# Performance work log

Hardware: AMD Instinct MI355X
Metric: run time of the kernel (lower is better)

## Reference

```python
import jax, jax.numpy as jnp
import numpy as np

B, S, D_MODEL, N_HEADS, D_HEAD = 2, 2048, 512, 8, 64
AMBIENT_K = -1.0
EPS = 1e-7


def log_map_origin(x, K):
    """Lorentz log map at origin, curvature K<0. x: (..., d+1) -> (..., d)."""
    c = -K
    sc = jnp.sqrt(c)
    x_t = x[..., :1]
    x_s = x[..., 1:]
    nrm = jnp.maximum(jnp.linalg.norm(x_s, axis=-1, keepdims=True), EPS)
    theta = jnp.arccosh(jnp.maximum(sc * x_t, 1.0 + EPS)) / sc  # geodesic distance
    return theta * x_s / nrm


def exp_map_batched(u, K_vals):
    """Per-head Lorentz exp map at origin. u: (B,S,H,dh), K_vals: (H,) negative.
    Returns (B,S,H,dh+1) with time component first."""
    c = (-K_vals)[None, None, :, None]          # (1,1,H,1)
    sc = jnp.sqrt(c)
    n = jnp.maximum(jnp.linalg.norm(u, axis=-1, keepdims=True), EPS)
    t = jnp.cosh(sc * n) / sc                   # time component
    s = jnp.sinh(sc * n) / (sc * n) * u         # space components
    return jnp.concatenate([t, s], axis=-1)


def setup_inputs() -> dict:
    key = jax.random.key(0)
    k_x, k_q, k_k, k_v, k_o = jax.random.split(key, 5)
    # Lorentz points on the K=-1 manifold: x_t = sqrt(1 + |x_s|^2)
    x_s = 0.5 * jax.random.normal(k_x, (B, S, D_MODEL), dtype=jnp.float32)
    x_t = jnp.sqrt(1.0 + jnp.sum(x_s * x_s, axis=-1, keepdims=True))
    x = jnp.concatenate([x_t, x_s], axis=-1)    # (B, S, d_model+1)
    scale = 1.0 / np.sqrt(D_MODEL)
    W_q = scale * jax.random.normal(k_q, (D_MODEL, N_HEADS * D_HEAD), dtype=jnp.float32)
    W_k = scale * jax.random.normal(k_k, (D_MODEL, N_HEADS * D_HEAD), dtype=jnp.float32)
    W_v = scale * jax.random.normal(k_v, (D_MODEL, N_HEADS * D_HEAD), dtype=jnp.float32)
    W_o = scale * jax.random.normal(k_o, (N_HEADS * D_HEAD, D_MODEL), dtype=jnp.float32)
    log_abs_K = jnp.zeros((N_HEADS,), dtype=jnp.float32)  # init_K = -1 -> log(1) = 0
    return {"x": x, "W_q": W_q, "W_k": W_k, "W_v": W_v, "W_o": W_o,
            "log_abs_K": log_abs_K}


def reference(x, W_q, W_k, W_v, W_o, log_abs_K):
    b, s, _ = x.shape
    K_vals = -jnp.exp(log_abs_K)                            # (H,) negative curvatures
    x_eu = log_map_origin(x, AMBIENT_K)                     # (B,S,D)
    Q = (x_eu @ W_q).reshape(b, s, N_HEADS, D_HEAD)
    Kp = (x_eu @ W_k).reshape(b, s, N_HEADS, D_HEAD)
    V = (x_eu @ W_v).reshape(b, s, N_HEADS, D_HEAD)
    Q_hyp = exp_map_batched(Q, K_vals).transpose(0, 2, 1, 3)   # (B,H,S,dh+1)
    K_hyp = exp_map_batched(Kp, K_vals).transpose(0, 2, 1, 3)
    V = V.transpose(0, 2, 1, 3)                                # (B,H,S,dh)
    Q_t, Q_s = Q_hyp[..., 0], Q_hyp[..., 1:]
    K_t, K_s = K_hyp[..., 0], K_hyp[..., 1:]
    # Lorentzian inner product: -q_t k_t + <q_s, k_s>
    lorentz_ip = (jnp.einsum('bhqd,bhkd->bhqk', Q_s, K_s)
                  - jnp.einsum('bhq,bhk->bhqk', Q_t, K_t))
    abs_K = jnp.exp(log_abs_K)[None, :, None, None]
    scores = abs_K * (-lorentz_ip) / np.sqrt(D_HEAD)           # (B,H,S,S)
    causal = jnp.triu(jnp.ones((s, s), dtype=bool), k=1)[None, None]
    scores = jnp.where(causal, -jnp.inf, scores)
    attn = jax.nn.softmax(scores, axis=-1)
    out = jnp.einsum('bhqk,bhkd->bhqd', attn, V)               # (B,H,S,dh)
    out = out.transpose(0, 2, 1, 3).reshape(b, s, N_HEADS * D_HEAD)
    return out @ W_o                                           # (B,S,D)
```

## Files before the change

### kernel.cpp

```cpp
#include <hip/hip_runtime.h>
#include <math.h>

#define S_LEN 2048
#define B_SZ 2
#define NH 8
#define DH 64
#define DM 512
#define MROWS 4096

typedef __attribute__((ext_vector_type(8))) short s16x8;
typedef __attribute__((ext_vector_type(4))) float fx4;
typedef __attribute__((ext_vector_type(16))) float fx16;
typedef __attribute__((ext_vector_type(4))) int ix4;
typedef __attribute__((ext_vector_type(2))) int ix2;

__device__ inline short f2bf(float x){
  unsigned u = __float_as_uint(x);
  u = (u + 0x7FFFu + ((u >> 16) & 1u)) >> 16;
  return (short)u;
}
__device__ inline float bf2f(short s){
  return __uint_as_float(((unsigned)(unsigned short)s) << 16);
}

__device__ inline fx4 mfma16(s16x8 a, s16x8 b, fx4 c){
  return __builtin_amdgcn_mfma_f32_16x16x32_bf16(a, b, c, 0, 0, 0);
}
__device__ inline fx16 mfma32(s16x8 a, s16x8 b, fx16 c){
  return __builtin_amdgcn_mfma_f32_32x32x16_bf16(a, b, c, 0, 0, 0);
}
__device__ inline int cvtpk(float a, float b){
  int r; asm("v_cvt_pk_bf16_f32 %0, %1, %2" : "=v"(r) : "v"(a), "v"(b)); return r;
}

#define GLL16(g, l) __builtin_amdgcn_global_load_lds((const __attribute__((address_space(1))) void*)(g), (__attribute__((address_space(3))) void*)(l), 16, 0, 0)
#define GLL4(g, l)  __builtin_amdgcn_global_load_lds((const __attribute__((address_space(1))) void*)(g), (__attribute__((address_space(3))) void*)(l), 4, 0, 0)

__global__ __launch_bounds__(256) void prep_kernel(const float* __restrict__ W0,
                                                   const float* __restrict__ W1,
                                                   const float* __restrict__ W2,
                                                   const float* __restrict__ W3,
                                                   short* __restrict__ Wt,
                                                   const float* __restrict__ x,
                                                   short* __restrict__ xeu){
  __shared__ short tile[64][66];
  int bid = blockIdx.x;
  int t = threadIdx.x;
  if (bid < 256){
    int z = bid >> 6, rem = bid & 63;
    const float* W = (z == 0) ? W0 : (z == 1) ? W1 : (z == 2) ? W2 : W3;
    short* Wtz = Wt + (size_t)z * DM * DM;
    int n0 = (rem & 7) * 64, k0 = (rem >> 3) * 64;
    int nl = t & 63;
    #pragma unroll
    for (int p = 0; p < 16; ++p){
      int kl = (t >> 6) + p * 4;
      tile[kl][nl] = f2bf(W[(size_t)(k0 + kl) * DM + n0 + nl]);
    }
    __syncthreads();
    int kl2 = t & 63;
    #pragma unroll
    for (int p = 0; p < 16; ++p){
      int nl2 = (t >> 6) + p * 4;
      Wtz[(size_t)(n0 + nl2) * DM + k0 + kl2] = tile[kl2][nl2];
    }
  } else {
    int row = (bid - 256) * 4 + (t >> 6);
    int lane = t & 63;
    const float* xr = x + (size_t)row * (DM + 1);
    float v[8]; float ss = 0.f;
    #pragma unroll
    for (int j = 0; j < 8; ++j){
      v[j] = xr[1 + lane * 8 + j];
      ss += v[j] * v[j];
    }
    #pragma unroll
    for (int off = 1; off < 64; off <<= 1) ss += __shfl_xor(ss, off);
    float nrm = sqrtf(ss);
    float xt = xr[0];
    float theta = acoshf(fmaxf(xt, 1.0f + 1e-7f));
    float scl = theta / fmaxf(nrm, 1e-7f);
    s16x8 pk;
    #pragma unroll
    for (int j = 0; j < 8; ++j) pk[j] = f2bf(scl * v[j]);
    *(s16x8*)(xeu + (size_t)row * DM + lane * 8) = pk;
  }
}

__global__ __launch_bounds__(256, 2) void gemm_fused_kernel(const short* __restrict__ A,
                                                            const short* __restrict__ Bt,
                                                            const float* __restrict__ labsK,
                                                            float* __restrict__ Qt,
                                                            short* __restrict__ Qs,
                                                            float* __restrict__ Kt,
                                                            short* __restrict__ Ks,
                                                            short* __restrict__ Vt){
  __shared__ __attribute__((aligned(16))) short Stage[4][8192];
  const int K = DM;
  int z = blockIdx.z;
  int hp = blockIdx.y;
  int n0 = hp * 128, m0 = blockIdx.x * 128;
  int t = threadIdx.x;
  int w = t >> 6, lane = t & 63;
  int wm = w >> 1, wn = w & 1;
  int lg = lane >> 4, lr = lane & 15;
  const short* Btz = Bt + (size_t)z * K * DM;

  int coff[4]; const short* asrcp[4]; const short* bsrcp[4];
  #pragma unroll
  for (int j = 0; j < 4; ++j){
    int ch = t + 256 * j;
    int r = ch >> 3, c = ch & 7;
    coff[j] = ch * 8;
    asrcp[j] = A   + (size_t)(m0 + r) * K + 8 * (c ^ (r & 7));
    bsrcp[j] = Btz + (size_t)(n0 + r) * K + 8 * (c ^ (r & 7));
  }

  #pragma unroll
  for (int j = 0; j < 4; ++j){
    GLL16(asrcp[j], &Stage[0][coff[j]]);
    GLL16(bsrcp[j], &Stage[2][coff[j]]);
  }

  fx4 acc[4][4] = {};
  for (int ks = 0; ks < 4; ++ks){
    ;
    break;
  }
  for (int ks = 0; ks < 8; ++ks){
    asm volatile("s_waitcnt vmcnt(0)" ::: "memory");
    __builtin_amdgcn_s_barrier();
    if (ks < 7){
      int nb = (ks + 1) & 1;
      int kk = (ks + 1) * 64;
      #pragma unroll
      for (int j = 0; j < 4; ++j){
        GLL16(asrcp[j] + kk, &Stage[nb][coff[j]]);
        GLL16(bsrcp[j] + kk, &Stage[2 + nb][coff[j]]);
      }
    }
    int buf = ks & 1;
    s16x8 af[4][2], bf[4][2];
    #pragma unroll
    for (int mi = 0; mi < 4; ++mi){
      int row = wm * 64 + mi * 16 + lr;
      #pragma unroll
      for (int s = 0; s < 2; ++s)
        af[mi][s] = *(const s16x8*)&Stage[buf][row * 64 + ((4 * s + lg) ^ (row & 7)) * 8];
    }
    #pragma unroll
    for (int ni = 0; ni < 4; ++ni){
      int row = wn * 64 + ni * 16 + lr;
      #pragma unroll
      for (int s = 0; s < 2; ++s)
        bf[ni][s] = *(const s16x8*)&Stage[2 + buf][row * 64 + ((4 * s + lg) ^ (row & 7)) * 8];
    }
    __builtin_amdgcn_s_setprio(1);
    #pragma unroll
    for (int s = 0; s < 2; ++s)
      #pragma unroll
      for (int mi = 0; mi < 4; ++mi)
        #pragma unroll
        for (int ni = 0; ni < 4; ++ni)
          acc[mi][ni] = mfma16(af[mi][s], bf[ni][s], acc[mi][ni]);
    __builtin_amdgcn_s_setprio(0);
  }

  int h = hp * 2 + wn;
  if (z < 2){
    float c  = __expf(labsK[h]);
    float sc = sqrtf(c);
    float invsc = __frcp_rn(sc);
    float a  = 0.125f * c * 1.4426950408889634f;
    float tmul = (z == 0) ? a : 1.0f;
    float vmul = (z == 0) ? -a : 1.0f;
    float* Tt = (z == 0) ? Qt : Kt;
    short* Ts = (z == 0) ? Qs : Ks;
    #pragma unroll
    for (int mi = 0; mi < 4; ++mi)
      #pragma unroll
      for (int r = 0; r < 4; ++r){
        float prt = 0.f;
        #pragma unroll
        for (int ni = 0; ni < 4; ++ni) prt += acc[mi][ni][r] * acc[mi][ni][r];
        prt += __shfl_xor(prt, 1);
        prt += __shfl_xor(prt, 2);
        prt += __shfl_xor(prt, 4);
        prt += __shfl_xor(prt, 8);
        float n = fmaxf(sqrtf(prt), 1e-7f);
        float arg = sc * n;
        float e = __expf(arg), ei = __frcp_rn(e);
        float tval = tmul * 0.5f * (e + ei) * invsc;
        float vscl = vmul * 0.5f * (e - ei) * __frcp_rn(arg);
        int grow = m0 + wm * 64 + mi * 16 + 4 * lg + r;
        int b = grow >> 11, s = grow & (S_LEN - 1);
        size_t bhs = ((size_t)(b * NH + h) * S_LEN + s);
        if (lr == 0) Tt[bhs] = tval;
        #pragma unroll
        for (int ni = 0; ni < 4; ++ni)
          Ts[bhs * DH + ni * 16 + lr] = f2bf(vscl * acc[mi][ni][r]);
      }
  } else {
    __syncthreads();
    short* vt = &Stage[0][0] + w * 4352;
    #pragma unroll
    for (int mi = 0; mi < 4; ++mi)
      #pragma unroll
      for (int ni = 0; ni < 4; ++ni)
        #pragma unroll
        for (int r = 0; r < 4; ++r)
          vt[(ni * 16 + lr) * 68 + mi * 16 + 4 * lg + r] = f2bf(acc[mi][ni][r]);
    int b = m0 >> 11;
    int sglob = (m0 & (S_LEN - 1)) + wm * 64;
    size_t vbase = ((size_t)(b * NH + h) * DH + lane) * S_LEN + sglob;
    #pragma unroll
    for (int j = 0; j < 8; ++j){
      s16x8 val = *(const s16x8*)&vt[lane * 68 + j * 8];
      *(s16x8*)(Vt + vbase + j * 8) = val;
    }
  }
}

__global__ __launch_bounds__(256, 3) void attn_kernel(const short* __restrict__ Qs,
                                                      const float* __restrict__ Qt,
                                                      const short* __restrict__ Ks,
                                                      const float* __restrict__ Kt,
                                                      const short* __restrict__ Vt,
                                                      float* __restrict__ Mpart,
                                                      float* __restrict__ Lpart,
                                                      short* __restrict__ Obn,
                                                      short* __restrict__ Obf){
  __shared__ __attribute__((aligned(16))) short Ksm[3][4096];
  __shared__ __attribute__((aligned(16))) short Vsm[3][4096];
  __shared__ __attribute__((aligned(16))) float Ktm[3][64];

  int bx = blockIdx.x;
  int bh = bx & 15;
  int id = bx >> 4;
  int g, c;
  if (id < 4)       { g = id;                 c = 0; }
  else if (id < 12) { g = 4 + ((id - 4) >> 1);  c = (id - 4) & 1; }
  else if (id < 24) { int r = id - 12; int q3 = r / 3; g = 8 + q3; c = r - 3 * q3; }
  else              { g = 12 + ((id - 24) >> 2); c = (id - 24) & 3; }
  int nch = (g >> 2) + 1;
  int kbeg = 512 * c;
  int kend = 512 * c + 512; { int ge = 128 * g + 128; if (ge < kend) kend = ge; }
  int ntc = (kend - kbeg) >> 6;

  int tid = threadIdx.x;
  int w = tid >> 6, lane = tid & 63;
  int l5 = lane & 31, hi = lane >> 5;
  size_t bhS = (size_t)bh * S_LEN;

  const short* Kg  = Ks + bhS * DH;
  const short* Vg  = Vt + (size_t)bh * DH * S_LEN;
  const float* Ktg = Kt + bhS;

  int srow = lane >> 3;
  int scol = ((lane & 7) * 8) ^ (srow << 3);
  const short* kg0 = Kg + (size_t)(kbeg + 16 * w + srow) * DH + scol;
  const short* kg1 = kg0 + 8 * DH;
  const short* vg0 = Vg + (size_t)(16 * w + srow) * S_LEN + kbeg + scol;
  const short* vg1 = vg0 + 8 * S_LEN;
  const float* ktg = Ktg + kbeg + lane;

  int q0w = 128 * g + 32 * w;
  int q   = q0w + l5;
  int qmax = q0w + 31;
  s16x8 qf[4];
  #pragma unroll
  for (int dblk = 0; dblk < 4; ++dblk)
    qf[dblk] = *(const s16x8*)(Qs + (bhS + q) * DH + dblk * 16 + hi * 8);
  float aqt = Qt[bhS + q];

  fx16 acc0, acc1;
  #pragma unroll
  for (int i = 0; i < 16; ++i){ acc0[i] = 0.f; acc1[i] = 0.f; }
  float mrun = 0.f, lrun = 0.f;

  #define STAGE_T(tt, b) { int off_ = (tt) * 64; \
    GLL16(kg0 + (size_t)off_ * DH, &Ksm[b][16 * w * 64]); \
    GLL16(kg1 + (size_t)off_ * DH, &Ksm[b][16 * w * 64 + 512]); \
    GLL16(vg0 + off_, &Vsm[b][16 * w * 64]); \
    GLL16(vg1 + off_, &Vsm[b][16 * w * 64 + 512]); \
    if (w == 3) GLL4(ktg + off_, &Ktm[b][0]); }

  STAGE_T(0, 0);
  if (ntc > 1) STAGE_T(1, 1);

  int buf = 0, sbuf = 2;
  for (int t = 0; t < ntc; ++t){
    int k0 = kbeg + t * 64;
    if (t + 1 < ntc){
      if (w == 3) asm volatile("s_waitcnt vmcnt(5)" ::: "memory");
      else        asm volatile("s_waitcnt vmcnt(4)" ::: "memory");
    } else {
      asm volatile("s_waitcnt vmcnt(0)" ::: "memory");
    }
    __builtin_amdgcn_s_barrier();
    if (t + 2 < ntc) STAGE_T(t + 2, sbuf);

    if (k0 <= qmax){
      fx16 st[2];
      __builtin_amdgcn_s_setprio(1);
      #pragma unroll
      for (int s = 0; s < 2; ++s){
        const short* kb = &Ksm[buf][(32 * s + l5) * 64];
        fx16 z;
        #pragma unroll
        for (int i = 0; i < 16; ++i) z[i] = 0.f;
        #pragma unroll
        for (int dblk = 0; dblk < 4; ++dblk){
          s16x8 kf = *(const s16x8*)(kb + ((16 * dblk + 8 * hi) ^ ((l5 & 7) << 3)));
          z = mfma32(kf, qf[dblk], z);
        }
        st[s] = z;
      }
      __builtin_amdgcn_s_setprio(0);
      float p[2][16];
      #pragma unroll
      for (int s = 0; s < 2; ++s)
        #pragma unroll
        for (int m4 = 0; m4 < 4; ++m4){
          fx4 kt4 = *(const fx4*)&Ktm[buf][32 * s + 8 * m4 + 4 * hi];
          #pragma unroll
          for (int tt = 0; tt < 4; ++tt)
            p[s][4 * m4 + tt] = st[s][4 * m4 + tt] + aqt * kt4[tt];
        }
      if (k0 + 63 > q0w){
        #pragma unroll
        for (int s = 0; s < 2; ++s)
          #pragma unroll
          for (int r = 0; r < 16; ++r){
            int kg2 = k0 + 32 * s + (r & 3) + 8 * (r >> 2) + 4 * hi;
            if (kg2 > q) p[s][r] = -3e38f;
          }
      }
      float v16[16];
      #pragma unroll
      for (int i = 0; i < 16; ++i) v16[i] = fmaxf(p[0][i], p[1][i]);
      #pragma unroll
      for (int i = 0; i < 8; ++i) v16[i] = fmaxf(v16[i], v16[i + 8]);
      #pragma unroll
      for (int i = 0; i < 4; ++i) v16[i] = fmaxf(v16[i], v16[i + 4]);
      float pmax = fmaxf(fmaxf(v16[0], v16[1]), fmaxf(v16[2], v16[3]));
      pmax = fmaxf(pmax, __shfl_xor(pmax, 32));
      if (!__all(pmax <= mrun + 8.f)){
        float mnew = fmaxf(mrun, pmax);
        float scl = __builtin_amdgcn_exp2f(mrun - mnew);
        mrun = mnew;
        lrun *= scl;
        #pragma unroll
        for (int i = 0; i < 16; ++i){ acc0[i] *= scl; acc1[i] *= scl; }
      }
      float sm[16];
      #pragma unroll
      for (int i = 0; i < 16; ++i){
        p[0][i] = __builtin_amdgcn_exp2f(p[0][i] - mrun);
        p[1][i] = __builtin_amdgcn_exp2f(p[1][i] - mrun);
        sm[i] = p[0][i] + p[1][i];
      }
      #pragma unroll
      for (int i = 0; i < 8; ++i) sm[i] += sm[i + 8];
      #pragma unroll
      for (int i = 0; i < 4; ++i) sm[i] += sm[i + 4];
      float rsum = (sm[0] + sm[1]) + (sm[2] + sm[3]);
      rsum += __shfl_xor(rsum, 32);
      lrun += rsum;

      #pragma unroll
      for (int h = 0; h < 4; ++h){
        int s = h >> 1, hb = h & 1;
        int w0 = cvtpk(p[s][8 * hb + 0], p[s][8 * hb + 1]);
        int w1 = cvtpk(p[s][8 * hb + 2], p[s][8 * hb + 3]);
        int w2 = cvtpk(p[s][8 * hb + 4], p[s][8 * hb + 5]);
        int w3 = cvtpk(p[s][8 * hb + 6], p[s][8 * hb + 7]);
        int sdA = hi ? w0 : w2;
        int sdB = hi ? w1 : w3;
        int rcA = __shfl_xor(sdA, 32);
        int rcB = __shfl_xor(sdB, 32);
        ix4 fw;
        fw.x = hi ? rcA : w0; fw.y = hi ? rcB : w1;
        fw.z = hi ? w2 : rcA; fw.w = hi ? w3 : rcB;
        s16x8 pf = __builtin_bit_cast(s16x8, fw);
        const short* vb0 = &Vsm[buf][(l5) * 64 + ((16 * h + 8 * hi) ^ ((l5 & 7) << 3))];
        const short* vb1 = vb0 + 32 * 64;
        s16x8 vf0 = *(const s16x8*)vb0;
        s16x8 vf1 = *(const s16x8*)vb1;
        __builtin_amdgcn_s_setprio(1);
        acc0 = mfma32(vf0, pf, acc0);
        acc1 = mfma32(vf1, pf, acc1);
        __builtin_amdgcn_s_setprio(0);
      }
    }
    buf  = (buf == 2)  ? 0 : buf + 1;
    sbuf = (sbuf == 2) ? 0 : sbuf + 1;
  }

  float invl = 1.0f / lrun;
  int qi = 32 * w + l5;
  if (nch == 1){
    int bb = bh >> 3, hh = bh & 7;
    short* orow = Obf + ((size_t)bb * S_LEN + 128 * g + qi) * DM + hh * DH;
    #pragma unroll
    for (int j = 0; j < 4; ++j){
      ix2 v0, v1;
      v0.x = cvtpk(acc0[4 * j + 0] * invl, acc0[4 * j + 1] * invl);
      v0.y = cvtpk(acc0[4 * j + 2] * invl, acc0[4 * j + 3] * invl);
      v1.x = cvtpk(acc1[4 * j + 0] * invl, acc1[4 * j + 1] * invl);
      v1.y = cvtpk(acc1[4 * j + 2] * invl, acc1[4 * j + 3] * invl);
      *(ix2*)(orow + 8 * j + 4 * hi)      = v0;
      *(ix2*)(orow + 32 + 8 * j + 4 * hi) = v1;
    }
  } else {
    int slot = ((bh << 4) + g) * 4 + c;
    if (hi == 0){
      Mpart[(size_t)slot * 128 + qi] = mrun;
      Lpart[(size_t)slot * 128 + qi] = lrun;
    }
    short* Op = Obn + (size_t)slot * 8192 + (size_t)qi * 64;
    #pragma unroll
    for (int j = 0; j < 4; ++j){
      ix2 v0, v1;
      v0.x = cvtpk(acc0[4 * j + 0] * invl, acc0[4 * j + 1] * invl);
      v0.y = cvtpk(acc0[4 * j + 2] * invl, acc0[4 * j + 3] * invl);
      v1.x = cvtpk(acc1[4 * j + 0] * invl, acc1[4 * j + 1] * invl);
      v1.y = cvtpk(acc1[4 * j + 2] * invl, acc1[4 * j + 3] * invl);
      *(ix2*)(Op + 8 * j + 4 * hi)      = v0;
      *(ix2*)(Op + 32 + 8 * j + 4 * hi) = v1;
    }
  }
}

__global__ __launch_bounds__(256) void combine_kernel(const float* __restrict__ Mpart,
                                                      const float* __restrict__ Lpart,
                                                      const short* __restrict__ Obn,
                                                      short* __restrict__ Obf){
  int bx = blockIdx.x;
  int bhg = bx % 192;
  int qq = bx / 192;
  int bh = bhg & 15;
  int g = 4 + (bhg >> 4);
  int t = threadIdx.x;
  int q = qq * 32 + (t >> 3);
  int oct = t & 7;
  int nch = (g >> 2) + 1;
  int gbase = ((bh << 4) + g) * 4;

  float mc[4], lc[4];
  #pragma unroll
  for (int c = 0; c < 4; ++c){
    mc[c] = Mpart[(size_t)(gbase + c) * 128 + q];
    lc[c] = Lpart[(size_t)(gbase + c) * 128 + q];
    if (c >= nch) mc[c] = -3e38f;
  }
  float M = fmaxf(fmaxf(mc[0], mc[1]), fmaxf(mc[2], mc[3]));
  float ww[4]; float D = 0.f;
  #pragma unroll
  for (int c = 0; c < 4; ++c){
    ww[c] = __builtin_amdgcn_exp2f(mc[c] - M) * lc[c];
    if (c >= nch) ww[c] = 0.f;
    D += ww[c];
  }
  float invD = 1.f / D;
  #pragma unroll
  for (int c = 0; c < 4; ++c) ww[c] *= invD;

  const short* ob = Obn + (size_t)gbase * 8192 + (size_t)q * 64 + oct * 8;
  float accf[8] = {0.f,0.f,0.f,0.f,0.f,0.f,0.f,0.f};
  #pragma unroll
  for (int c = 0; c < 4; ++c){
    s16x8 v = *(const s16x8*)(ob + (size_t)c * 8192);
    #pragma unroll
    for (int i = 0; i < 8; ++i) accf[i] += ww[c] * bf2f(v[i]);
  }
  s16x8 pk;
  #pragma unroll
  for (int dd = 0; dd < 8; ++dd) pk[dd] = f2bf(accf[dd]);
  int bb = bh >> 3, hh = bh & 7;
  *(s16x8*)(Obf + ((size_t)bb * S_LEN + 128 * g + q) * DM + hh * DH + oct * 8) = pk;
}

__global__ __launch_bounds__(256, 4) void gemm_o_kernel(const short* __restrict__ A,
                                                        const short* __restrict__ Bt,
                                                        float* __restrict__ C){
  __shared__ __attribute__((aligned(16))) short Asm[2][64 * 64];
  __shared__ __attribute__((aligned(16))) short Bsm[2][64 * 64];
  const int K = DM;
  int n0 = blockIdx.y * 64, m0 = blockIdx.x * 64;
  int t = threadIdx.x;
  int w = t >> 6, lane = t & 63;
  int wm = w >> 1, wn = w & 1;
  int lg = lane >> 4, lr = lane & 15;

  int aoff[2]; const short* asrcp[2];
  int boff[2]; const short* bsrcp[2];
  #pragma unroll
  for (int j = 0; j < 2; ++j){
    int ch = t + 256 * j;
    int r = ch >> 3, c = ch & 7;
    aoff[j] = ch * 8;
    asrcp[j] = A + (size_t)(m0 + r) * K + 8 * (c ^ (r & 7));
    boff[j] = ch * 8;
    bsrcp[j] = Bt + (size_t)(n0 + r) * K + 8 * (c ^ (r & 7));
  }

  {
    short* ab = &Asm[0][0]; short* bb = &Bsm[0][0];
    #pragma unroll
    for (int j = 0; j < 2; ++j){ GLL16(asrcp[j], ab + aoff[j]); GLL16(bsrcp[j], bb + boff[j]); }
  }

  fx4 acc[2][2] = {};
  for (int ks = 0; ks < 8; ++ks){
    asm volatile("s_waitcnt vmcnt(0)" ::: "memory");
    __builtin_amdgcn_s_barrier();
    if (ks < 7){
      int nb = (ks + 1) & 1;
      short* ab = &Asm[nb][0]; short* bb = &Bsm[nb][0];
      int kk = (ks + 1) * 64;
      #pragma unroll
      for (int j = 0; j < 2; ++j){ GLL16(asrcp[j] + kk, ab + aoff[j]); GLL16(bsrcp[j] + kk, bb + boff[j]); }
    }
    int buf = ks & 1;
    s16x8 af[2][2], bf[2][2];
    #pragma unroll
    for (int mi = 0; mi < 2; ++mi){
      int row = wm * 32 + mi * 16 + lr;
      #pragma unroll
      for (int s = 0; s < 2; ++s)
        af[mi][s] = *(const s16x8*)&Asm[buf][row * 64 + ((4 * s + lg) ^ (row & 7)) * 8];
    }
    #pragma unroll
    for (int ni = 0; ni < 2; ++ni){
      int row = wn * 32 + ni * 16 + lr;
      #pragma unroll
      for (int s = 0; s < 2; ++s)
        bf[ni][s] = *(const s16x8*)&Bsm[buf][row * 64 + ((4 * s + lg) ^ (row & 7)) * 8];
    }
    __builtin_amdgcn_s_setprio(1);
    #pragma unroll
    for (int s = 0; s < 2; ++s)
      #pragma unroll
      for (int mi = 0; mi < 2; ++mi)
        #pragma unroll
        for (int ni = 0; ni < 2; ++ni)
          acc[mi][ni] = mfma16(af[mi][s], bf[ni][s], acc[mi][ni]);
    __builtin_amdgcn_s_setprio(0);
  }

  #pragma unroll
  for (int mi = 0; mi < 2; ++mi)
    #pragma unroll
    for (int ni = 0; ni < 2; ++ni)
      #pragma unroll
      for (int r = 0; r < 4; ++r){
        int row = m0 + wm * 32 + mi * 16 + 4 * lg + r;
        int col = n0 + wn * 32 + ni * 16 + lr;
        C[(size_t)row * DM + col] = acc[mi][ni][r];
      }
}

extern "C" void kernel_launch(void* const* d_in, const int* in_sizes, int n_in,
                              void* d_out, int out_size, void* d_ws, size_t ws_size,
                              hipStream_t stream) {
  const float* x     = (const float*)d_in[0];
  const float* Wq    = (const float*)d_in[1];
  const float* Wk    = (const float*)d_in[2];
  const float* Wv    = (const float*)d_in[3];
  const float* Wo    = (const float*)d_in[4];
  const float* labsK = (const float*)d_in[5];

  char* w = (char*)d_ws;
  short* Wt    = (short*)(w);
  short* xeu   = (short*)(w + (2ull  << 20));
  short* Qs    = (short*)(w + (30ull << 20));
  short* Ks    = (short*)(w + (34ull << 20));
  short* Vt    = (short*)(w + (38ull << 20));
  float* Qt    = (float*)(w + (42ull << 20));
  float* Kt    = (float*)(w + (42ull << 20) + (128ull << 10));
  short* Obf   = (short*)(w + (42ull << 20) + (256ull << 10));
  short* Obn   = (short*)(w + (48ull << 20));
  float* Mpart = (float*)(w + (80ull << 20));
  float* Lpart = (float*)(w + (81ull << 20));

  prep_kernel<<<dim3(1280), 256, 0, stream>>>(Wq, Wk, Wv, Wo, Wt, x, xeu);

  gemm_fused_kernel<<<dim3(32, 4, 3), 256, 0, stream>>>(
      xeu, Wt, labsK, Qt, Qs, Kt, Ks, Vt);

  attn_kernel<<<dim3(640), 256, 0, stream>>>(
      Qs, Qt, Ks, Kt, Vt, Mpart, Lpart, Obn, Obf);

  combine_kernel<<<dim3(768), 256, 0, stream>>>(Mpart, Lpart, Obn, Obf);

  gemm_o_kernel<<<dim3(64, 8), 256, 0, stream>>>(Obf, Wt + 3 * DM * DM, (float*)d_out);
}
```

Before: 59.86 us.

## Replace split-K attention plus combine with 64-query blocks scheduled longest-first

The attention kernel no longer splits long causal rows into key chunks with partial max/sum outputs merged by a separate combine kernel. Each block now has 128 threads (2 waves) handling 64 queries over all causal key tiles, with blocks ordered so the longest query groups launch first. This removes the combine launch and the partial-result global traffic, at the cost of longer serial loops for late query blocks and less parallelism per row. The new block size also doubles the K/V staging loads per wave and changes the wait counts to match.

```diff
diff --git a/kernel.cpp b/kernel.cpp
--- a/kernel.cpp
+++ b/kernel.cpp
@@ -18,9 +18,6 @@
   unsigned u = __float_as_uint(x);
   u = (u + 0x7FFFu + ((u >> 16) & 1u)) >> 16;
   return (short)u;
-}
-__device__ inline float bf2f(short s){
-  return __uint_as_float(((unsigned)(unsigned short)s) << 16);
 }
 
 __device__ inline fx4 mfma16(s16x8 a, s16x8 b, fx4 c){
@@ -77,8 +74,7 @@
     #pragma unroll
     for (int off = 1; off < 64; off <<= 1) ss += __shfl_xor(ss, off);
     float nrm = sqrtf(ss);
-    float xt = xr[0];
-    float theta = acoshf(fmaxf(xt, 1.0f + 1e-7f));
+    float theta = acoshf(fmaxf(xr[0], 1.0f + 1e-7f));
     float scl = theta / fmaxf(nrm, 1e-7f);
     s16x8 pk;
     #pragma unroll
@@ -123,10 +119,6 @@
   }
 
   fx4 acc[4][4] = {};
-  for (int ks = 0; ks < 4; ++ks){
-    ;
-    break;
-  }
   for (int ks = 0; ks < 8; ++ks){
     asm volatile("s_waitcnt vmcnt(0)" ::: "memory");
     __builtin_amdgcn_s_barrier();
@@ -221,14 +213,11 @@
   }
 }
 
-__global__ __launch_bounds__(256, 3) void attn_kernel(const short* __restrict__ Qs,
+__global__ __launch_bounds__(128, 2) void attn_kernel(const short* __restrict__ Qs,
                                                       const float* __restrict__ Qt,
                                                       const short* __restrict__ Ks,
                                                       const float* __restrict__ Kt,
                                                       const short* __restrict__ Vt,
-                                                      float* __restrict__ Mpart,
-                                                      float* __restrict__ Lpart,
-                                                      short* __restrict__ Obn,
                                                       short* __restrict__ Obf){
   __shared__ __attribute__((aligned(16))) short Ksm[3][4096];
   __shared__ __attribute__((aligned(16))) short Vsm[3][4096];
@@ -236,16 +225,8 @@
 
   int bx = blockIdx.x;
   int bh = bx & 15;
-  int id = bx >> 4;
-  int g, c;
-  if (id < 4)       { g = id;                 c = 0; }
-  else if (id < 12) { g = 4 + ((id - 4) >> 1);  c = (id - 4) & 1; }
-  else if (id < 24) { int r = id - 12; int q3 = r / 3; g = 8 + q3; c = r - 3 * q3; }
-  else              { g = 12 + ((id - 24) >> 2); c = (id - 24) & 3; }
-  int nch = (g >> 2) + 1;
-  int kbeg = 512 * c;
-  int kend = 512 * c + 512; { int ge = 128 * g + 128; if (ge < kend) kend = ge; }
-  int ntc = (kend - kbeg) >> 6;
+  int g  = 31 - (bx >> 4);
+  int ntc = g + 1;
 
   int tid = threadIdx.x;
   int w = tid >> 6, lane = tid & 63;
@@ -258,15 +239,12 @@
 
   int srow = lane >> 3;
   int scol = ((lane & 7) * 8) ^ (srow << 3);
-  const short* kg0 = Kg + (size_t)(kbeg + 16 * w + srow) * DH + scol;
-  const short* kg1 = kg0 + 8 * DH;
-  const short* vg0 = Vg + (size_t)(16 * w + srow) * S_LEN + kbeg + scol;
-  const short* vg1 = vg0 + 8 * S_LEN;
-  const float* ktg = Ktg + kbeg + lane;
-
-  int q0w = 128 * g + 32 * w;
+  const short* kgA = Kg + (size_t)(32 * w + srow) * DH + scol;
+  const short* vgA = Vg + (size_t)(32 * w + srow) * S_LEN + scol;
+  const float* ktg = Ktg + lane;
+
+  int q0w = 64 * g + 32 * w;
   int q   = q0w + l5;
-  int qmax = q0w + 31;
   s16x8 qf[4];
   #pragma unroll
   for (int dblk = 0; dblk < 4; ++dblk)
@@ -279,28 +257,32 @@
   float mrun = 0.f, lrun = 0.f;
 
   #define STAGE_T(tt, b) { int off_ = (tt) * 64; \
-    GLL16(kg0 + (size_t)off_ * DH, &Ksm[b][16 * w * 64]); \
-    GLL16(kg1 + (size_t)off_ * DH, &Ksm[b][16 * w * 64 + 512]); \
-    GLL16(vg0 + off_, &Vsm[b][16 * w * 64]); \
-    GLL16(vg1 + off_, &Vsm[b][16 * w * 64 + 512]); \
-    if (w == 3) GLL4(ktg + off_, &Ktm[b][0]); }
+    GLL16(kgA + (size_t)off_ * DH,           &Ksm[b][(32 * w +  0) * 64]); \
+    GLL16(kgA + (size_t)off_ * DH +  8 * DH, &Ksm[b][(32 * w +  8) * 64]); \
+    GLL16(kgA + (size_t)off_ * DH + 16 * DH, &Ksm[b][(32 * w + 16) * 64]); \
+    GLL16(kgA + (size_t)off_ * DH + 24 * DH, &Ksm[b][(32 * w + 24) * 64]); \
+    GLL16(vgA + off_,              &Vsm[b][(32 * w +  0) * 64]); \
+    GLL16(vgA + off_ +  8 * S_LEN, &Vsm[b][(32 * w +  8) * 64]); \
+    GLL16(vgA + off_ + 16 * S_LEN, &Vsm[b][(32 * w + 16) * 64]); \
+    GLL16(vgA + off_ + 24 * S_LEN, &Vsm[b][(32 * w + 24) * 64]); \
+    if (w == 1) GLL4(ktg + off_, &Ktm[b][0]); }
 
   STAGE_T(0, 0);
   if (ntc > 1) STAGE_T(1, 1);
 
   int buf = 0, sbuf = 2;
   for (int t = 0; t < ntc; ++t){
-    int k0 = kbeg + t * 64;
+    int k0 = t * 64;
     if (t + 1 < ntc){
-      if (w == 3) asm volatile("s_waitcnt vmcnt(5)" ::: "memory");
-      else        asm volatile("s_waitcnt vmcnt(4)" ::: "memory");
+      if (w == 1) asm volatile("s_waitcnt vmcnt(9)" ::: "memory");
+      else        asm volatile("s_waitcnt vmcnt(8)" ::: "memory");
     } else {
       asm volatile("s_waitcnt vmcnt(0)" ::: "memory");
     }
     __builtin_amdgcn_s_barrier();
     if (t + 2 < ntc) STAGE_T(t + 2, sbuf);
 
-    if (k0 <= qmax){
+    {
       fx16 st[2];
       __builtin_amdgcn_s_setprio(1);
       #pragma unroll
@@ -369,8 +351,8 @@
       lrun += rsum;
 
       #pragma unroll
-      for (int h = 0; h < 4; ++h){
-        int s = h >> 1, hb = h & 1;
+      for (int h2 = 0; h2 < 4; ++h2){
+        int s = h2 >> 1, hb = h2 & 1;
         int w0 = cvtpk(p[s][8 * hb + 0], p[s][8 * hb + 1]);
         int w1 = cvtpk(p[s][8 * hb + 2], p[s][8 * hb + 3]);
         int w2 = cvtpk(p[s][8 * hb + 4], p[s][8 * hb + 5]);
@@ -383,7 +365,7 @@
         fw.x = hi ? rcA : w0; fw.y = hi ? rcB : w1;
         fw.z = hi ? w2 : rcA; fw.w = hi ? w3 : rcB;
         s16x8 pf = __builtin_bit_cast(s16x8, fw);
-        const short* vb0 = &Vsm[buf][(l5) * 64 + ((16 * h + 8 * hi) ^ ((l5 & 7) << 3))];
+        const short* vb0 = &Vsm[buf][(l5) * 64 + ((16 * h2 + 8 * hi) ^ ((l5 & 7) << 3))];
         const short* vb1 = vb0 + 32 * 64;
         s16x8 vf0 = *(const s16x8*)vb0;
         s16x8 vf1 = *(const s16x8*)vb1;
@@ -396,89 +378,22 @@
     buf  = (buf == 2)  ? 0 : buf + 1;
     sbuf = (sbuf == 2) ? 0 : sbuf + 1;
   }
+  #undef STAGE_T
 
   float invl = 1.0f / lrun;
   int qi = 32 * w + l5;
-  if (nch == 1){
-    int bb = bh >> 3, hh = bh & 7;
-    short* orow = Obf + ((size_t)bb * S_LEN + 128 * g + qi) * DM + hh * DH;
-    #pragma unroll
-    for (int j = 0; j < 4; ++j){
-      ix2 v0, v1;
-      v0.x = cvtpk(acc0[4 * j + 0] * invl, acc0[4 * j + 1] * invl);
-      v0.y = cvtpk(acc0[4 * j + 2] * invl, acc0[4 * j + 3] * invl);
-      v1.x = cvtpk(acc1[4 * j + 0] * invl, acc1[4 * j + 1] * invl);
-      v1.y = cvtpk(acc1[4 * j + 2] * invl, acc1[4 * j + 3] * invl);
-      *(ix2*)(orow + 8 * j + 4 * hi)      = v0;
-      *(ix2*)(orow + 32 + 8 * j + 4 * hi) = v1;
-    }
-  } else {
-    int slot = ((bh << 4) + g) * 4 + c;
-    if (hi == 0){
-      Mpart[(size_t)slot * 128 + qi] = mrun;
-      Lpart[(size_t)slot * 128 + qi] = lrun;
-    }
-    short* Op = Obn + (size_t)slot * 8192 + (size_t)qi * 64;
-    #pragma unroll
-    for (int j = 0; j < 4; ++j){
-      ix2 v0, v1;
-      v0.x = cvtpk(acc0[4 * j + 0] * invl, acc0[4 * j + 1] * invl);
-      v0.y = cvtpk(acc0[4 * j + 2] * invl, acc0[4 * j + 3] * invl);
-      v1.x = cvtpk(acc1[4 * j + 0] * invl, acc1[4 * j + 1] * invl);
-      v1.y = cvtpk(acc1[4 * j + 2] * invl, acc1[4 * j + 3] * invl);
-      *(ix2*)(Op + 8 * j + 4 * hi)      = v0;
-      *(ix2*)(Op + 32 + 8 * j + 4 * hi) = v1;
-    }
-  }
-}
-
-__global__ __launch_bounds__(256) void combine_kernel(const float* __restrict__ Mpart,
-                                                      const float* __restrict__ Lpart,
-                                                      const short* __restrict__ Obn,
-                                                      short* __restrict__ Obf){
-  int bx = blockIdx.x;
-  int bhg = bx % 192;
-  int qq = bx / 192;
-  int bh = bhg & 15;
-  int g = 4 + (bhg >> 4);
-  int t = threadIdx.x;
-  int q = qq * 32 + (t >> 3);
-  int oct = t & 7;
-  int nch = (g >> 2) + 1;
-  int gbase = ((bh << 4) + g) * 4;
-
-  float mc[4], lc[4];
-  #pragma unroll
-  for (int c = 0; c < 4; ++c){
-    mc[c] = Mpart[(size_t)(gbase + c) * 128 + q];
-    lc[c] = Lpart[(size_t)(gbase + c) * 128 + q];
-    if (c >= nch) mc[c] = -3e38f;
-  }
-  float M = fmaxf(fmaxf(mc[0], mc[1]), fmaxf(mc[2], mc[3]));
-  float ww[4]; float D = 0.f;
-  #pragma unroll
-  for (int c = 0; c < 4; ++c){
-    ww[c] = __builtin_amdgcn_exp2f(mc[c] - M) * lc[c];
-    if (c >= nch) ww[c] = 0.f;
-    D += ww[c];
-  }
-  float invD = 1.f / D;
-  #pragma unroll
-  for (int c = 0; c < 4; ++c) ww[c] *= invD;
-
-  const short* ob = Obn + (size_t)gbase * 8192 + (size_t)q * 64 + oct * 8;
-  float accf[8] = {0.f,0.f,0.f,0.f,0.f,0.f,0.f,0.f};
-  #pragma unroll
-  for (int c = 0; c < 4; ++c){
-    s16x8 v = *(const s16x8*)(ob + (size_t)c * 8192);
-    #pragma unroll
-    for (int i = 0; i < 8; ++i) accf[i] += ww[c] * bf2f(v[i]);
-  }
-  s16x8 pk;
-  #pragma unroll
-  for (int dd = 0; dd < 8; ++dd) pk[dd] = f2bf(accf[dd]);
   int bb = bh >> 3, hh = bh & 7;
-  *(s16x8*)(Obf + ((size_t)bb * S_LEN + 128 * g + q) * DM + hh * DH + oct * 8) = pk;
+  short* orow = Obf + ((size_t)bb * S_LEN + 64 * g + qi) * DM + hh * DH;
+  #pragma unroll
+  for (int j = 0; j < 4; ++j){
+    ix2 v0, v1;
+    v0.x = cvtpk(acc0[4 * j + 0] * invl, acc0[4 * j + 1] * invl);
+    v0.y = cvtpk(acc0[4 * j + 2] * invl, acc0[4 * j + 3] * invl);
+    v1.x = cvtpk(acc1[4 * j + 0] * invl, acc1[4 * j + 1] * invl);
+    v1.y = cvtpk(acc1[4 * j + 2] * invl, acc1[4 * j + 3] * invl);
+    *(ix2*)(orow + 8 * j + 4 * hi)      = v0;
+    *(ix2*)(orow + 32 + 8 * j + 4 * hi) = v1;
+  }
 }
 
 __global__ __launch_bounds__(256, 4) void gemm_o_kernel(const short* __restrict__ A,
@@ -580,19 +495,13 @@
   float* Qt    = (float*)(w + (42ull << 20));
   float* Kt    = (float*)(w + (42ull << 20) + (128ull << 10));
   short* Obf   = (short*)(w + (42ull << 20) + (256ull << 10));
-  short* Obn   = (short*)(w + (48ull << 20));
-  float* Mpart = (float*)(w + (80ull << 20));
-  float* Lpart = (float*)(w + (81ull << 20));
 
   prep_kernel<<<dim3(1280), 256, 0, stream>>>(Wq, Wk, Wv, Wo, Wt, x, xeu);
 
   gemm_fused_kernel<<<dim3(32, 4, 3), 256, 0, stream>>>(
       xeu, Wt, labsK, Qt, Qs, Kt, Ks, Vt);
 
-  attn_kernel<<<dim3(640), 256, 0, stream>>>(
-      Qs, Qt, Ks, Kt, Vt, Mpart, Lpart, Obn, Obf);
-
-  combine_kernel<<<dim3(768), 256, 0, stream>>>(Mpart, Lpart, Obn, Obf);
+  attn_kernel<<<dim3(512), 128, 0, stream>>>(Qs, Qt, Ks, Kt, Vt, Obf);
 
   gemm_o_kernel<<<dim3(64, 8), 256, 0, stream>>>(Obf, Wt + 3 * DM * DM, (float*)d_out);
 }
```

After: 82.82 us. +38.4%, slower.

## Split attention KV into 256-wide chunks and switch to double-buffered staging

Applied to the files above, without the earlier changes.

The attention split-K work decomposition changes from 512-key chunks to 256-key chunks, with a closed-form triangular mapping from block id to query group and chunk. The grid grows from 640 to 1152 blocks and occupancy rises to 4 blocks per CU. LDS staging drops from triple to double buffering with an extra barrier per tile, freeing shared memory for the added occupancy. The combine kernel now covers more query groups and merges a variable number of partials with an online rescaling loop. The aims are better load balance and more parallelism in the causal attention, at the cost of more partial writes, combine traffic and synchronisation.

```diff
diff --git a/kernel.cpp b/kernel.cpp
--- a/kernel.cpp
+++ b/kernel.cpp
@@ -77,8 +77,7 @@
     #pragma unroll
     for (int off = 1; off < 64; off <<= 1) ss += __shfl_xor(ss, off);
     float nrm = sqrtf(ss);
-    float xt = xr[0];
-    float theta = acoshf(fmaxf(xt, 1.0f + 1e-7f));
+    float theta = acoshf(fmaxf(xr[0], 1.0f + 1e-7f));
     float scl = theta / fmaxf(nrm, 1e-7f);
     s16x8 pk;
     #pragma unroll
@@ -123,10 +122,6 @@
   }
 
   fx4 acc[4][4] = {};
-  for (int ks = 0; ks < 4; ++ks){
-    ;
-    break;
-  }
   for (int ks = 0; ks < 8; ++ks){
     asm volatile("s_waitcnt vmcnt(0)" ::: "memory");
     __builtin_amdgcn_s_barrier();
@@ -221,7 +216,7 @@
   }
 }
 
-__global__ __launch_bounds__(256, 3) void attn_kernel(const short* __restrict__ Qs,
+__global__ __launch_bounds__(256, 4) void attn_kernel(const short* __restrict__ Qs,
                                                       const float* __restrict__ Qt,
                                                       const short* __restrict__ Ks,
                                                       const float* __restrict__ Kt,
@@ -230,21 +225,21 @@
                                                       float* __restrict__ Lpart,
                                                       short* __restrict__ Obn,
                                                       short* __restrict__ Obf){
-  __shared__ __attribute__((aligned(16))) short Ksm[3][4096];
-  __shared__ __attribute__((aligned(16))) short Vsm[3][4096];
-  __shared__ __attribute__((aligned(16))) float Ktm[3][64];
+  __shared__ __attribute__((aligned(16))) short Ksm[2][4096];
+  __shared__ __attribute__((aligned(16))) short Vsm[2][4096];
+  __shared__ __attribute__((aligned(16))) float Ktm[2][64];
 
   int bx = blockIdx.x;
   int bh = bx & 15;
   int id = bx >> 4;
-  int g, c;
-  if (id < 4)       { g = id;                 c = 0; }
-  else if (id < 12) { g = 4 + ((id - 4) >> 1);  c = (id - 4) & 1; }
-  else if (id < 24) { int r = id - 12; int q3 = r / 3; g = 8 + q3; c = r - 3 * q3; }
-  else              { g = 12 + ((id - 24) >> 2); c = (id - 24) & 3; }
-  int nch = (g >> 2) + 1;
-  int kbeg = 512 * c;
-  int kend = 512 * c + 512; { int ge = 128 * g + 128; if (ge < kend) kend = ge; }
+  int g = (int)(2.0f * __fsqrt_rn((float)(id + 1))) - 1;
+  if (g < 0) g = 0;
+  while (((g + 2) * (g + 2)) / 4 <= id) ++g;
+  while (((g + 1) * (g + 1)) / 4 > id) --g;
+  int c = id - ((g + 1) * (g + 1)) / 4;
+  int nch = (g + 2) >> 1;
+  int kbeg = 256 * c;
+  int kend = 256 * c + 256; { int ge = 128 * (g + 1); if (ge < kend) kend = ge; }
   int ntc = (kend - kbeg) >> 6;
 
   int tid = threadIdx.x;
@@ -266,7 +261,6 @@
 
   int q0w = 128 * g + 32 * w;
   int q   = q0w + l5;
-  int qmax = q0w + 31;
   s16x8 qf[4];
   #pragma unroll
   for (int dblk = 0; dblk < 4; ++dblk)
@@ -288,7 +282,6 @@
   STAGE_T(0, 0);
   if (ntc > 1) STAGE_T(1, 1);
 
-  int buf = 0, sbuf = 2;
   for (int t = 0; t < ntc; ++t){
     int k0 = kbeg + t * 64;
     if (t + 1 < ntc){
@@ -298,9 +291,9 @@
       asm volatile("s_waitcnt vmcnt(0)" ::: "memory");
     }
     __builtin_amdgcn_s_barrier();
-    if (t + 2 < ntc) STAGE_T(t + 2, sbuf);
-
-    if (k0 <= qmax){
+    int buf = t & 1;
+
+    {
       fx16 st[2];
       __builtin_amdgcn_s_setprio(1);
       #pragma unroll
@@ -369,8 +362,8 @@
       lrun += rsum;
 
       #pragma unroll
-      for (int h = 0; h < 4; ++h){
-        int s = h >> 1, hb = h & 1;
+      for (int h2 = 0; h2 < 4; ++h2){
+        int s = h2 >> 1, hb = h2 & 1;
         int w0 = cvtpk(p[s][8 * hb + 0], p[s][8 * hb + 1]);
         int w1 = cvtpk(p[s][8 * hb + 2], p[s][8 * hb + 3]);
         int w2 = cvtpk(p[s][8 * hb + 4], p[s][8 * hb + 5]);
@@ -383,7 +376,7 @@
         fw.x = hi ? rcA : w0; fw.y = hi ? rcB : w1;
         fw.z = hi ? w2 : rcA; fw.w = hi ? w3 : rcB;
         s16x8 pf = __builtin_bit_cast(s16x8, fw);
-        const short* vb0 = &Vsm[buf][(l5) * 64 + ((16 * h + 8 * hi) ^ ((l5 & 7) << 3))];
+        const short* vb0 = &Vsm[buf][(l5) * 64 + ((16 * h2 + 8 * hi) ^ ((l5 & 7) << 3))];
         const short* vb1 = vb0 + 32 * 64;
         s16x8 vf0 = *(const s16x8*)vb0;
         s16x8 vf1 = *(const s16x8*)vb1;
@@ -393,9 +386,10 @@
         __builtin_amdgcn_s_setprio(0);
       }
     }
-    buf  = (buf == 2)  ? 0 : buf + 1;
-    sbuf = (sbuf == 2) ? 0 : sbuf + 1;
-  }
+    __builtin_amdgcn_s_barrier();
+    if (t + 2 < ntc) STAGE_T(t + 2, buf);
+  }
+  #undef STAGE_T
 
   float invl = 1.0f / lrun;
   int qi = 32 * w + l5;
@@ -413,7 +407,7 @@
       *(ix2*)(orow + 32 + 8 * j + 4 * hi) = v1;
     }
   } else {
-    int slot = ((bh << 4) + g) * 4 + c;
+    int slot = bh * 72 + id;
     if (hi == 0){
       Mpart[(size_t)slot * 128 + qi] = mrun;
       Lpart[(size_t)slot * 128 + qi] = lrun;
@@ -437,46 +431,34 @@
                                                       const short* __restrict__ Obn,
                                                       short* __restrict__ Obf){
   int bx = blockIdx.x;
-  int bhg = bx % 192;
-  int qq = bx / 192;
+  int bhg = bx % 224;
+  int qq = bx / 224;
   int bh = bhg & 15;
-  int g = 4 + (bhg >> 4);
+  int g = 2 + (bhg >> 4);
   int t = threadIdx.x;
   int q = qq * 32 + (t >> 3);
   int oct = t & 7;
-  int nch = (g >> 2) + 1;
-  int gbase = ((bh << 4) + g) * 4;
-
-  float mc[4], lc[4];
-  #pragma unroll
-  for (int c = 0; c < 4; ++c){
-    mc[c] = Mpart[(size_t)(gbase + c) * 128 + q];
-    lc[c] = Lpart[(size_t)(gbase + c) * 128 + q];
-    if (c >= nch) mc[c] = -3e38f;
-  }
-  float M = fmaxf(fmaxf(mc[0], mc[1]), fmaxf(mc[2], mc[3]));
-  float ww[4]; float D = 0.f;
-  #pragma unroll
-  for (int c = 0; c < 4; ++c){
-    ww[c] = __builtin_amdgcn_exp2f(mc[c] - M) * lc[c];
-    if (c >= nch) ww[c] = 0.f;
-    D += ww[c];
-  }
-  float invD = 1.f / D;
-  #pragma unroll
-  for (int c = 0; c < 4; ++c) ww[c] *= invD;
-
-  const short* ob = Obn + (size_t)gbase * 8192 + (size_t)q * 64 + oct * 8;
-  float accf[8] = {0.f,0.f,0.f,0.f,0.f,0.f,0.f,0.f};
-  #pragma unroll
-  for (int c = 0; c < 4; ++c){
-    s16x8 v = *(const s16x8*)(ob + (size_t)c * 8192);
-    #pragma unroll
-    for (int i = 0; i < 8; ++i) accf[i] += ww[c] * bf2f(v[i]);
-  }
+  int nch = (g + 2) >> 1;
+  int base = bh * 72 + ((g + 1) * (g + 1)) / 4;
+
+  float Mr = -3e38f, Dr = 0.f;
+  float acc[8] = {0.f,0.f,0.f,0.f,0.f,0.f,0.f,0.f};
+  for (int c = 0; c < nch; ++c){
+    float m = Mpart[(size_t)(base + c) * 128 + q];
+    float l = Lpart[(size_t)(base + c) * 128 + q];
+    float Mn = fmaxf(Mr, m);
+    float sOld = __builtin_amdgcn_exp2f(Mr - Mn);
+    float sNew = __builtin_amdgcn_exp2f(m - Mn) * l;
+    s16x8 v = *(const s16x8*)(Obn + (size_t)(base + c) * 8192 + (size_t)q * 64 + oct * 8);
+    #pragma unroll
+    for (int i = 0; i < 8; ++i) acc[i] = acc[i] * sOld + sNew * bf2f(v[i]);
+    Dr = Dr * sOld + sNew;
+    Mr = Mn;
+  }
+  float invD = 1.f / Dr;
   s16x8 pk;
   #pragma unroll
-  for (int dd = 0; dd < 8; ++dd) pk[dd] = f2bf(accf[dd]);
+  for (int dd = 0; dd < 8; ++dd) pk[dd] = f2bf(acc[dd] * invD);
   int bb = bh >> 3, hh = bh & 7;
   *(s16x8*)(Obf + ((size_t)bb * S_LEN + 128 * g + q) * DM + hh * DH + oct * 8) = pk;
 }
@@ -589,10 +571,10 @@
   gemm_fused_kernel<<<dim3(32, 4, 3), 256, 0, stream>>>(
       xeu, Wt, labsK, Qt, Qs, Kt, Ks, Vt);
 
-  attn_kernel<<<dim3(640), 256, 0, stream>>>(
+  attn_kernel<<<dim3(1152), 256, 0, stream>>>(
       Qs, Qt, Ks, Kt, Vt, Mpart, Lpart, Obn, Obf);
 
-  combine_kernel<<<dim3(768), 256, 0, stream>>>(Mpart, Lpart, Obn, Obf);
+  combine_kernel<<<dim3(896), 256, 0, stream>>>(Mpart, Lpart, Obn, Obf);
 
   gemm_o_kernel<<<dim3(64, 8), 256, 0, stream>>>(Obf, Wt + 3 * DM * DM, (float*)d_out);
 }
```

New measurement: 60.61 us. Within noise of the previous version (+1.3%).
